# Kernel optimization log

Measured on AMD Instinct MI355X. Metric: run time of the kernel, lower is better.

Reference implementation:

```python
import jax, jax.numpy as jnp
import numpy as np

B, S, D, H = 4, 2048, 1024, 16
DH = D // H  # head dim = 64
MASK_VALUE = -1000000.0


def setup_inputs() -> dict:
    key = jax.random.key(0)
    ks = jax.random.split(key, 8)
    return {
        "key": jax.random.normal(ks[0], (B, S, D), jnp.float32),
        "query": jax.random.normal(ks[1], (B, S, D), jnp.float32),
        "value": jax.random.normal(ks[2], (B, S, D), jnp.float32),
        "valid_lens": jax.random.randint(ks[3], (B,), 0, 2048, jnp.int32),
        # nn.Linear weights stored as [out_features, in_features]
        "Wk": jax.random.normal(ks[4], (D, D), jnp.float32) / np.sqrt(D),
        "Wq": jax.random.normal(ks[5], (D, D), jnp.float32) / np.sqrt(D),
        "Wv": jax.random.normal(ks[6], (D, D), jnp.float32) / np.sqrt(D),
        "Wo": jax.random.normal(ks[7], (D, D), jnp.float32) / np.sqrt(D),
    }


def _split_heads(x):
    # [B, S, D] -> [B, H, S, DH]
    return x.reshape(B, S, H, DH).transpose(0, 2, 1, 3)


def reference(key, query, value, valid_lens, Wk, Wq, Wv, Wo):
    # projections (Linear: x @ W^T, bias=False)
    q = _split_heads(query @ Wq.T)  # [B, H, S, DH]
    k = _split_heads(key @ Wk.T)
    v = _split_heads(value @ Wv.T)

    scale = 1.0 / jnp.sqrt(jnp.asarray(DH, q.dtype))
    scores = jnp.einsum("bhqd,bhkd->bhqk", q, k) * scale  # [B, H, S, S]

    # valid_lens masks the key axis per batch element (same for all heads/queries)
    key_mask = jnp.arange(S) < valid_lens[:, None]  # [B, S]
    scores = jnp.where(key_mask[:, None, None, :], scores, MASK_VALUE)

    attn = jax.nn.softmax(scores, axis=-1)
    out = jnp.einsum("bhqk,bhkd->bhqd", attn, v)  # [B, H, S, DH]
    out = out.transpose(0, 2, 1, 3).reshape(B, S, D)  # concat heads
    return out @ Wo.T
```

## Files before the change

### kernel.cpp

```cpp
#include <hip/hip_runtime.h>
#include <hip/hip_bf16.h>
#include <stdint.h>

typedef __bf16 bf16;
typedef __bf16 bf16x4 __attribute__((ext_vector_type(4)));
typedef __bf16 bf16x8 __attribute__((ext_vector_type(8)));
typedef float f32x4 __attribute__((ext_vector_type(4)));
typedef float f32x8 __attribute__((ext_vector_type(8)));

#define MFMA16 __builtin_amdgcn_mfma_f32_16x16x32_bf16

__device__ __forceinline__ void gload_lds16(void* lds, const void* g) {
  __builtin_amdgcn_global_load_lds(
      (const __attribute__((address_space(1))) unsigned int*)g,
      (__attribute__((address_space(3))) unsigned int*)lds, 16, 0, 0);
}
__device__ __forceinline__ void gload_lds4(void* lds, const void* g) {
  __builtin_amdgcn_global_load_lds(
      (const __attribute__((address_space(1))) unsigned int*)g,
      (__attribute__((address_space(3))) unsigned int*)lds, 4, 0, 0);
}

#define S_BARRIER() __builtin_amdgcn_s_barrier()
#define SCHED_FENCE() __builtin_amdgcn_sched_barrier(0)
#define WAIT_LGKM0()                                   \
  do {                                                 \
    asm volatile("s_waitcnt lgkmcnt(0)" ::: "memory"); \
    __builtin_amdgcn_sched_barrier(0);                 \
  } while (0)
#define WAIT_VM(n) asm volatile("s_waitcnt vmcnt(" #n ")" ::: "memory")

__global__ __launch_bounds__(256) void cvt3(
    const float* __restrict__ s0, const float* __restrict__ s1,
    const float* __restrict__ s2, bf16* __restrict__ d0,
    bf16* __restrict__ d1, bf16* __restrict__ d2) {
  const float* srcs[3] = {s0, s1, s2};
  bf16* dsts[3] = {d0, d1, d2};
  const float* src = srcs[blockIdx.y];
  bf16* dst = dsts[blockIdx.y];
  int i = (blockIdx.x * 256 + threadIdx.x) * 4;
  f32x4 v = *(const f32x4*)(src + i);
  bf16x4 o;
#pragma unroll
  for (int j = 0; j < 4; j++) o[j] = (bf16)v[j];
  *(bf16x4*)(dst + i) = o;
}

__global__ __launch_bounds__(256) void cvt1(const float* __restrict__ src,
                                            bf16* __restrict__ dst) {
  int i = (blockIdx.x * 256 + threadIdx.x) * 4;
  f32x4 v = *(const f32x4*)(src + i);
  bf16x4 o;
#pragma unroll
  for (int j = 0; j < 4; j++) o[j] = (bf16)v[j];
  *(bf16x4*)(dst + i) = o;
}

__global__ __launch_bounds__(256) void cvt4(const float* __restrict__ w0,
                                            const float* __restrict__ w1,
                                            const float* __restrict__ w2,
                                            const float* __restrict__ w3,
                                            bf16* __restrict__ dst) {
  const float* srcs[4] = {w0, w1, w2, w3};
  const float* src = srcs[blockIdx.y];
  int i = (blockIdx.x * 256 + threadIdx.x) * 4;
  f32x4 v = *(const f32x4*)(src + i);
  bf16x4 o;
#pragma unroll
  for (int j = 0; j < 4; j++) o[j] = (bf16)v[j];
  *(bf16x4*)(dst + (size_t)blockIdx.y * 1048576 + i) = o;
}

__device__ __forceinline__ void gemmF_body(const bf16* __restrict__ A,
                                           const bf16* __restrict__ W,
                                           void* __restrict__ Craw, int mode,
                                           int m0, int n0, bf16* smem) {
  constexpr int K = 1024;
  const int t = threadIdx.x;
  const int lane = t & 63;
  const int m16 = lane & 15;
  const int quad = (lane >> 4) & 3;
  const int sw = m16 & 7;
  const int w = t >> 6;
  const int wm = (w >> 2) * 64;
  const int wn = (w & 3) * 64;

  const bf16* Ab = A + (size_t)m0 * K;
  const bf16* Bb = W + (size_t)n0 * K;

  auto STG = [&](int buf, int kt) {
    bf16* dA = smem + buf * 24576;
    bf16* dB = dA + 8192;
    const bf16* sA = Ab + kt * 64;
    const bf16* sB = Bb + kt * 64;
#pragma unroll
    for (int ld = 0; ld < 2; ld++) {
      int idx = ld * 512 + t;
      int row = idx >> 3;
      int c = (idx & 7) ^ (row & 7);
      gload_lds16(dA + idx * 8, sA + (size_t)row * K + c * 8);
    }
#pragma unroll
    for (int ld = 0; ld < 4; ld++) {
      int idx = ld * 512 + t;
      int row = idx >> 3;
      int c = (idx & 7) ^ (row & 7);
      gload_lds16(dB + idx * 8, sB + (size_t)row * K + c * 8);
    }
  };

  bf16x8 aR[8], bR[8];
  auto LD = [&](int buf) {
    const bf16* As = smem + buf * 24576;
    const bf16* Bs = As + 8192;
#pragma unroll
    for (int f = 0; f < 4; f++)
#pragma unroll
      for (int ks = 0; ks < 2; ks++) {
        aR[f * 2 + ks] = *(const bf16x8*)&As[(wm + f * 16 + m16) * 64 +
                                             (((ks * 4 + quad) ^ sw) * 8)];
        bR[f * 2 + ks] = *(const bf16x8*)&Bs[(wn + f * 16 + m16) * 64 +
                                             (((ks * 4 + quad) ^ sw) * 8)];
      }
  };

  f32x4 acc[4][4];
#pragma unroll
  for (int f = 0; f < 4; f++)
#pragma unroll
    for (int g = 0; g < 4; g++) acc[f][g] = (f32x4){0.f, 0.f, 0.f, 0.f};

  auto MM = [&]() {
    __builtin_amdgcn_s_setprio(1);
#pragma unroll
    for (int f = 0; f < 4; f++)
#pragma unroll
      for (int g = 0; g < 4; g++)
#pragma unroll
        for (int ks = 0; ks < 2; ks++)
          acc[f][g] = MFMA16(aR[f * 2 + ks], bR[g * 2 + ks], acc[f][g], 0, 0, 0);
    __builtin_amdgcn_s_setprio(0);
  };

  STG(0, 0);
  STG(1, 1);
  WAIT_VM(6);
  S_BARRIER();

  int bufR = 0;
#pragma unroll 1
  for (int kt = 0; kt < 14; ++kt) {
    LD(bufR);
    int bufS = bufR + 2;
    if (bufS >= 3) bufS -= 3;
    STG(bufS, kt + 2);
    S_BARRIER();
    WAIT_LGKM0();
    MM();
    WAIT_VM(6);
    S_BARRIER();
    bufR = (bufR + 1 == 3) ? 0 : bufR + 1;
  }
  LD(bufR);
  S_BARRIER();
  WAIT_LGKM0();
  MM();
  WAIT_VM(0);
  S_BARRIER();
  bufR = (bufR + 1 == 3) ? 0 : bufR + 1;
  LD(bufR);
  S_BARRIER();
  WAIT_LGKM0();
  MM();

#pragma unroll
  for (int f = 0; f < 4; f++) {
    int rbase = m0 + wm + f * 16 + quad * 4;
#pragma unroll
    for (int g = 0; g < 4; g++) {
      int col = n0 + wn + g * 16 + m16;
#pragma unroll
      for (int r = 0; r < 4; r++) {
        int row = rbase + r;
        if (mode == 0) {
          ((float*)Craw)[(size_t)row * 1024 + col] = acc[f][g][r];
        } else {
          int b = row >> 11, s = row & 2047;
          int h = col >> 6, d = col & 63;
          bf16 v = (bf16)acc[f][g][r];
          if (mode == 1)
            ((bf16*)Craw)[(((size_t)(b * 16 + h)) * 2048 + s) * 64 + d] = v;
          else
            ((bf16*)Craw)[(((size_t)(b * 16 + h)) * 64 + d) * 2048 + s] = v;
        }
      }
    }
  }
}

__global__ __launch_bounds__(512, 2) void gemm_qkv(
    const bf16* __restrict__ xq, const bf16* __restrict__ xk,
    const bf16* __restrict__ xv, const bf16* __restrict__ wb,
    const int* __restrict__ vlen, bf16* __restrict__ qp,
    bf16* __restrict__ kp, bf16* __restrict__ vt) {
  __shared__ bf16 smem[73728];
  const int m0 = blockIdx.y * 128;
  const int n0 = blockIdx.x * 256;
  const int z = blockIdx.z;
  if (z >= 1) {
    int b = m0 >> 11;
    int s0 = m0 & 2047;
    int vl = vlen[b];
    if (vl != 0 && s0 >= vl) return;
  }
  const bf16* A = (z == 0) ? xq : (z == 1) ? xk : xv;
  const bf16* W = wb + (size_t)z * 1048576;
  bf16* C = (z == 0) ? qp : (z == 1) ? kp : vt;
  gemmF_body(A, W, C, (z == 2) ? 2 : 1, m0, n0, smem);
}

__global__ __launch_bounds__(512, 2) void gemm_one(const bf16* __restrict__ A,
                                                   const bf16* __restrict__ W,
                                                   void* __restrict__ Craw,
                                                   int mode) {
  __shared__ bf16 smem[73728];
  gemmF_body(A, W, Craw, mode, blockIdx.y * 128, blockIdx.x * 256, smem);
}

template <int AF32, int WF32>
__global__ __launch_bounds__(256) void gemm_bt(const void* __restrict__ Araw,
                                               const void* __restrict__ Wraw,
                                               void* __restrict__ Craw,
                                               int mode) {
  constexpr int K = 1024;
  __shared__ bf16 As[128 * 32];
  __shared__ bf16 Bs[128 * 32];
  const int t = threadIdx.x;
  const int lane = t & 63;
  const int quad = lane >> 4;
  const int m16 = lane & 15;
  const int w = t >> 6;
  const int m0 = blockIdx.y * 128;
  const int n0 = blockIdx.x * 128;
  const int wm = (w >> 1) * 64;
  const int wn = (w & 1) * 64;

  f32x4 acc[4][4];
#pragma unroll
  for (int i = 0; i < 4; i++)
#pragma unroll
    for (int j = 0; j < 4; j++) acc[i][j] = (f32x4){0.f, 0.f, 0.f, 0.f};

  for (int kt = 0; kt < K / 32; kt++) {
    bf16x8 aR[2], bR[2];
#pragma unroll
    for (int p = 0; p < 2; p++) {
      int idx = p * 256 + t;
      int row = idx >> 2;
      int ce = (idx & 3) * 8;
      size_t aoff = (size_t)(m0 + row) * K + kt * 32 + ce;
      size_t boff = (size_t)(n0 + row) * K + kt * 32 + ce;
      if constexpr (AF32) {
        f32x8 av = *(const f32x8*)((const float*)Araw + aoff);
#pragma unroll
        for (int j = 0; j < 8; j++) aR[p][j] = (bf16)av[j];
      } else {
        aR[p] = *(const bf16x8*)((const bf16*)Araw + aoff);
      }
      if constexpr (WF32) {
        f32x8 bv = *(const f32x8*)((const float*)Wraw + boff);
#pragma unroll
        for (int j = 0; j < 8; j++) bR[p][j] = (bf16)bv[j];
      } else {
        bR[p] = *(const bf16x8*)((const bf16*)Wraw + boff);
      }
    }
    __syncthreads();
#pragma unroll
    for (int p = 0; p < 2; p++) {
      int idx = p * 256 + t;
      *(bf16x8*)&As[idx * 8] = aR[p];
      *(bf16x8*)&Bs[idx * 8] = bR[p];
    }
    __syncthreads();

    bf16x8 af[4], bfr[4];
#pragma unroll
    for (int i = 0; i < 4; i++) {
      af[i] = *(const bf16x8*)&As[(wm + i * 16 + m16) * 32 + quad * 8];
      bfr[i] = *(const bf16x8*)&Bs[(wn + i * 16 + m16) * 32 + quad * 8];
    }
#pragma unroll
    for (int i = 0; i < 4; i++)
#pragma unroll
      for (int j = 0; j < 4; j++)
        acc[i][j] = MFMA16(af[i], bfr[j], acc[i][j], 0, 0, 0);
  }

#pragma unroll
  for (int i = 0; i < 4; i++) {
    int rbase = m0 + wm + i * 16 + quad * 4;
#pragma unroll
    for (int j = 0; j < 4; j++) {
      int col = n0 + wn + j * 16 + m16;
#pragma unroll
      for (int r = 0; r < 4; r++) {
        int row = rbase + r;
        if (mode == 0) {
          ((float*)Craw)[(size_t)row * 1024 + col] = acc[i][j][r];
        } else {
          int b = row >> 11, s = row & 2047;
          int h = col >> 6, d = col & 63;
          bf16 v = (bf16)acc[i][j][r];
          if (mode == 1)
            ((bf16*)Craw)[(((size_t)(b * 16 + h)) * 2048 + s) * 64 + d] = v;
          else
            ((bf16*)Craw)[(((size_t)(b * 16 + h)) * 64 + d) * 2048 + s] = v;
        }
      }
    }
  }
}

__global__ __launch_bounds__(512, 2) void attn(const bf16* __restrict__ qp,
                                               const bf16* __restrict__ kp,
                                               const bf16* __restrict__ vt,
                                               const int* __restrict__ vlen,
                                               bf16* __restrict__ ctx) {
  __shared__ bf16 Ks[2][4096];
  __shared__ bf16 Vs[2][4096];

  const int t = threadIdx.x;
  const int lane = t & 63;
  const int quad = (lane >> 4) & 3;
  const int m16 = lane & 15;
  const int sw = m16 & 7;
  const int w = t >> 6;
  const int id = blockIdx.y * 8 + blockIdx.x;
  const int xcd = id & 7;
  const int j = id >> 3;
  const int bh = (j >> 3) * 8 + xcd;
  const int qt = j & 7;
  const int b = bh >> 4;
  const int h = bh & 15;
  const int vl = vlen[b];

  const float C1 = 0.18033688f;
  const float C2 = 46.166241f;
  const float sC1 = (vl == 0) ? 0.0f : C1;
  const float sC2 = (vl == 0) ? 0.0f : C2;

  bf16x8 qf[2][2];
#pragma unroll
  for (int a = 0; a < 2; a++) {
    const bf16* qb =
        qp + ((size_t)(bh * 2048 + qt * 256 + w * 32 + a * 16 + m16)) * 64;
    qf[a][0] = *(const bf16x8*)(qb + quad * 8);
    qf[a][1] = *(const bf16x8*)(qb + 32 + quad * 8);
  }

  float rsum[2] = {0.f, 0.f};
  f32x4 o[2][4];
#pragma unroll
  for (int a = 0; a < 2; a++)
#pragma unroll
    for (int nt = 0; nt < 4; nt++) o[a][nt] = (f32x4){0.f, 0.f, 0.f, 0.f};

  const int ktEnd = (vl == 0) ? 32 : ((vl + 63) >> 6);

  const int krow = t >> 3;
  const int kgc = (t & 7) ^ (krow & 7);
  auto STAGE = [&](int buf, int kt2) {
    gload_lds16(&Ks[buf][t * 8],
                &kp[((size_t)(bh * 2048 + kt2 * 64 + krow)) * 64 + kgc * 8]);
#pragma unroll
    for (int ld = 0; ld < 4; ld++) {
      int c = ld * 512 + t;
      int dh = c >> 5;
      int i4 = c & 31;
      int c8 = i4 >> 2;
      int jw = i4 & 3;
      int lc = c8 ^ (dh & 7);
      int slot = lc * 8 + jw * 2;
      int ks2 = slot >> 5;
      int w32 = slot & 31;
      int key = ks2 * 32 + ((w32 >> 2) & 1) * 16 + (w32 >> 3) * 4 + (w32 & 3);
      gload_lds4(&Vs[buf][c * 2],
                 &vt[((size_t)(bh * 64 + dh)) * 2048 + kt2 * 64 + key]);
    }
  };

  STAGE(0, 0);

  for (int kt = 0; kt < ktEnd; kt++) {
    const int cur = kt & 1;
    if (kt + 1 < ktEnd) {
      STAGE(cur ^ 1, kt + 1);
      WAIT_VM(5);
    } else {
      WAIT_VM(0);
    }
    S_BARRIER();
    SCHED_FENCE();
    const bf16* Ksb = Ks[cur];
    const bf16* Vsb = Vs[cur];

    f32x4 s[2][4];
#pragma unroll
    for (int a = 0; a < 2; a++)
#pragma unroll
      for (int nt = 0; nt < 4; nt++) s[a][nt] = (f32x4){0.f, 0.f, 0.f, 0.f};
#pragma unroll
    for (int nt = 0; nt < 4; nt++) {
#pragma unroll
      for (int ks = 0; ks < 2; ks++) {
        bf16x8 kf = *(const bf16x8*)&Ksb[(nt * 16 + m16) * 64 +
                                         (((ks * 4 + quad) ^ sw) * 8)];
        s[0][nt] = MFMA16(kf, qf[0][ks], s[0][nt], 0, 0, 0);
        s[1][nt] = MFMA16(kf, qf[1][ks], s[1][nt], 0, 0, 0);
      }
    }

    bf16x8 pa[2][2];
    const bool partial = (vl != 0) && (kt == (vl >> 6));
    if (!partial) {
#pragma unroll
      for (int a = 0; a < 2; a++)
#pragma unroll
        for (int nt = 0; nt < 4; nt++)
#pragma unroll
          for (int r = 0; r < 4; r++) {
            float p = __builtin_amdgcn_exp2f(s[a][nt][r] * sC1 - sC2);
            bf16 pb = (bf16)p;
            rsum[a] += (float)pb;
            pa[a][nt >> 1][(nt & 1) * 4 + r] = pb;
          }
    } else {
#pragma unroll
      for (int a = 0; a < 2; a++)
#pragma unroll
        for (int nt = 0; nt < 4; nt++) {
          int keyb = kt * 64 + nt * 16 + quad * 4;
#pragma unroll
          for (int r = 0; r < 4; r++) {
            float arg = (keyb + r >= vl) ? -12800.0f
                                         : (s[a][nt][r] * sC1 - sC2);
            float p = __builtin_amdgcn_exp2f(arg);
            bf16 pb = (bf16)p;
            rsum[a] += (float)pb;
            pa[a][nt >> 1][(nt & 1) * 4 + r] = pb;
          }
        }
    }

#pragma unroll
    for (int ks = 0; ks < 2; ks++) {
#pragma unroll
      for (int nt = 0; nt < 4; nt++) {
        bf16x8 vf = *(const bf16x8*)&Vsb[(nt * 16 + m16) * 64 +
                                         (((ks * 4 + quad) ^ sw) * 8)];
        o[0][nt] = MFMA16(pa[0][ks], vf, o[0][nt], 0, 0, 0);
        o[1][nt] = MFMA16(pa[1][ks], vf, o[1][nt], 0, 0, 0);
      }
    }
    S_BARRIER();
    SCHED_FENCE();
  }

#pragma unroll
  for (int a = 0; a < 2; a++) {
    rsum[a] += __shfl_xor(rsum[a], 16);
    rsum[a] += __shfl_xor(rsum[a], 32);
    rsum[a] = 1.0f / rsum[a];
  }

#pragma unroll
  for (int a = 0; a < 2; a++) {
#pragma unroll
    for (int r = 0; r < 4; r++) {
      float rr = __shfl(rsum[a], (lane & 48) | (quad * 4 + r));
#pragma unroll
      for (int nt = 0; nt < 4; nt++) {
        int dh = nt * 16 + m16;
        int sr = qt * 256 + w * 32 + a * 16 + quad * 4 + r;
        ctx[((size_t)(b * 2048 + sr)) * 1024 + h * 64 + dh] =
            (bf16)(o[a][nt][r] * rr);
      }
    }
  }
}

extern "C" void kernel_launch(void* const* d_in, const int* in_sizes, int n_in,
                              void* d_out, int out_size, void* d_ws,
                              size_t ws_size, hipStream_t stream) {
  const float* key = (const float*)d_in[0];
  const float* query = (const float*)d_in[1];
  const float* value = (const float*)d_in[2];
  const int* vlen = (const int*)d_in[3];
  const float* Wk = (const float*)d_in[4];
  const float* Wq = (const float*)d_in[5];
  const float* Wv = (const float*)d_in[6];
  const float* Wo = (const float*)d_in[7];

  const size_t NE = (size_t)4 * 2048 * 1024;
  const size_t WE = 1048576;

  const size_t needA = (6 * NE + 4 * WE) * sizeof(bf16);
  const size_t needB = (5 * NE + 4 * WE) * sizeof(bf16);
  dim3 gg(4, 64), gb(512), cb(256), ag(8, 64), ab(512);

  if (ws_size >= needA) {
    bf16* qp = (bf16*)d_ws;
    bf16* kp = qp + NE;
    bf16* vt = kp + NE;
    bf16* xq = vt + NE;
    bf16* xk = xq + NE;
    bf16* xv = xk + NE;
    bf16* wb = xv + NE;
    bf16* ctx = xq;

    cvt4<<<dim3(1024, 4), cb, 0, stream>>>(Wq, Wk, Wv, Wo, wb);
    cvt3<<<dim3(8192, 3), cb, 0, stream>>>(query, key, value, xq, xk, xv);
    gemm_qkv<<<dim3(4, 64, 3), gb, 0, stream>>>(xq, xk, xv, wb, vlen, qp, kp,
                                                vt);
    attn<<<ag, ab, 0, stream>>>(qp, kp, vt, vlen, ctx);
    gemm_one<<<gg, gb, 0, stream>>>(ctx, wb + 3 * WE, d_out, 0);
  } else if (ws_size >= needB) {
    bf16* qp = (bf16*)d_ws;
    bf16* kp = qp + NE;
    bf16* vt = kp + NE;
    bf16* ctx = vt + NE;
    bf16* xb = ctx + NE;
    bf16* wb = xb + NE;

    cvt4<<<dim3(1024, 4), cb, 0, stream>>>(Wq, Wk, Wv, Wo, wb);
    cvt1<<<8192, cb, 0, stream>>>(query, xb);
    gemm_one<<<gg, gb, 0, stream>>>(xb, wb + 0 * WE, qp, 1);
    cvt1<<<8192, cb, 0, stream>>>(key, xb);
    gemm_one<<<gg, gb, 0, stream>>>(xb, wb + 1 * WE, kp, 1);
    cvt1<<<8192, cb, 0, stream>>>(value, xb);
    gemm_one<<<gg, gb, 0, stream>>>(xb, wb + 2 * WE, vt, 2);
    attn<<<ag, ab, 0, stream>>>(qp, kp, vt, vlen, ctx);
    gemm_one<<<gg, gb, 0, stream>>>(ctx, wb + 3 * WE, d_out, 0);
  } else {
    bf16* qp = (bf16*)d_ws;
    bf16* kp = qp + NE;
    bf16* vt = kp + NE;
    bf16* ctx = vt + NE;
    dim3 g8(8, 64), b256(256);
    gemm_bt<1, 1><<<g8, b256, 0, stream>>>(query, Wq, qp, 1);
    gemm_bt<1, 1><<<g8, b256, 0, stream>>>(key, Wk, kp, 1);
    gemm_bt<1, 1><<<g8, b256, 0, stream>>>(value, Wv, vt, 2);
    attn<<<ag, ab, 0, stream>>>(qp, kp, vt, vlen, ctx);
    gemm_bt<0, 1><<<g8, b256, 0, stream>>>(ctx, Wo, d_out, 0);
  }
}
```

Before: 334.0 us.

## Triple-buffer K/V tiles, software-pipeline QK^T with softmax/PV, vectorize V staging

The attention kernel moves from double to triple LDS buffering and stages the next-next tile while it runs QK^T for tile kt+1 interleaved with the softmax and PV of tile kt, so MFMA work overlaps the exp computation. V staging drops the sixteen 4-byte global-to-LDS loads per thread in favor of one 16-byte load with XOR swizzling. PV then rebuilds each V fragment from two 4-element LDS reads. LDS use grows by half and register pressure rises from holding two score sets, which could hurt occupancy at launch_bounds(512,2).

```diff
diff --git a/kernel.cpp b/kernel.cpp
--- a/kernel.cpp
+++ b/kernel.cpp
@@ -14,11 +14,6 @@
   __builtin_amdgcn_global_load_lds(
       (const __attribute__((address_space(1))) unsigned int*)g,
       (__attribute__((address_space(3))) unsigned int*)lds, 16, 0, 0);
-}
-__device__ __forceinline__ void gload_lds4(void* lds, const void* g) {
-  __builtin_amdgcn_global_load_lds(
-      (const __attribute__((address_space(1))) unsigned int*)g,
-      (__attribute__((address_space(3))) unsigned int*)lds, 4, 0, 0);
 }
 
 #define S_BARRIER() __builtin_amdgcn_s_barrier()
@@ -327,8 +322,8 @@
                                                const bf16* __restrict__ vt,
                                                const int* __restrict__ vlen,
                                                bf16* __restrict__ ctx) {
-  __shared__ bf16 Ks[2][4096];
-  __shared__ bf16 Vs[2][4096];
+  __shared__ bf16 Ks[3][4096];
+  __shared__ bf16 Vs[3][4096];
 
   const int t = threadIdx.x;
   const int lane = t & 63;
@@ -338,17 +333,15 @@
   const int w = t >> 6;
   const int id = blockIdx.y * 8 + blockIdx.x;
   const int xcd = id & 7;
-  const int j = id >> 3;
-  const int bh = (j >> 3) * 8 + xcd;
-  const int qt = j & 7;
+  const int jj = id >> 3;
+  const int bh = (jj >> 3) * 8 + xcd;
+  const int qt = jj & 7;
   const int b = bh >> 4;
   const int h = bh & 15;
   const int vl = vlen[b];
 
-  const float C1 = 0.18033688f;
-  const float C2 = 46.166241f;
-  const float sC1 = (vl == 0) ? 0.0f : C1;
-  const float sC2 = (vl == 0) ? 0.0f : C2;
+  const float sC1 = (vl == 0) ? 0.0f : 0.18033688f;
+  const float sC2 = (vl == 0) ? 0.0f : 46.166241f;
 
   bf16x8 qf[2][2];
 #pragma unroll
@@ -368,60 +361,35 @@
 
   const int ktEnd = (vl == 0) ? 32 : ((vl + 63) >> 6);
 
-  const int krow = t >> 3;
-  const int kgc = (t & 7) ^ (krow & 7);
+  const int srow = t >> 3;
+  const int sgc = (t & 7) ^ (srow & 7);
   auto STAGE = [&](int buf, int kt2) {
     gload_lds16(&Ks[buf][t * 8],
-                &kp[((size_t)(bh * 2048 + kt2 * 64 + krow)) * 64 + kgc * 8]);
-#pragma unroll
-    for (int ld = 0; ld < 4; ld++) {
-      int c = ld * 512 + t;
-      int dh = c >> 5;
-      int i4 = c & 31;
-      int c8 = i4 >> 2;
-      int jw = i4 & 3;
-      int lc = c8 ^ (dh & 7);
-      int slot = lc * 8 + jw * 2;
-      int ks2 = slot >> 5;
-      int w32 = slot & 31;
-      int key = ks2 * 32 + ((w32 >> 2) & 1) * 16 + (w32 >> 3) * 4 + (w32 & 3);
-      gload_lds4(&Vs[buf][c * 2],
-                 &vt[((size_t)(bh * 64 + dh)) * 2048 + kt2 * 64 + key]);
-    }
-  };
-
-  STAGE(0, 0);
-
-  for (int kt = 0; kt < ktEnd; kt++) {
-    const int cur = kt & 1;
-    if (kt + 1 < ktEnd) {
-      STAGE(cur ^ 1, kt + 1);
-      WAIT_VM(5);
-    } else {
-      WAIT_VM(0);
-    }
-    S_BARRIER();
-    SCHED_FENCE();
-    const bf16* Ksb = Ks[cur];
-    const bf16* Vsb = Vs[cur];
-
-    f32x4 s[2][4];
+                &kp[((size_t)(bh * 2048 + kt2 * 64 + srow)) * 64 + sgc * 8]);
+    gload_lds16(&Vs[buf][t * 8],
+                &vt[((size_t)(bh * 64 + srow)) * 2048 + kt2 * 64 + sgc * 8]);
+  };
+
+  f32x4 s[2][4], sN[2][4];
+
+  auto QKT = [&](int buf, f32x4 (&sv)[2][4]) {
 #pragma unroll
     for (int a = 0; a < 2; a++)
 #pragma unroll
-      for (int nt = 0; nt < 4; nt++) s[a][nt] = (f32x4){0.f, 0.f, 0.f, 0.f};
+      for (int nt = 0; nt < 4; nt++) sv[a][nt] = (f32x4){0.f, 0.f, 0.f, 0.f};
 #pragma unroll
     for (int nt = 0; nt < 4; nt++) {
 #pragma unroll
       for (int ks = 0; ks < 2; ks++) {
-        bf16x8 kf = *(const bf16x8*)&Ksb[(nt * 16 + m16) * 64 +
-                                         (((ks * 4 + quad) ^ sw) * 8)];
-        s[0][nt] = MFMA16(kf, qf[0][ks], s[0][nt], 0, 0, 0);
-        s[1][nt] = MFMA16(kf, qf[1][ks], s[1][nt], 0, 0, 0);
-      }
-    }
-
-    bf16x8 pa[2][2];
+        bf16x8 kf = *(const bf16x8*)&Ks[buf][(nt * 16 + m16) * 64 +
+                                            (((ks * 4 + quad) ^ sw) * 8)];
+        sv[0][nt] = MFMA16(kf, qf[0][ks], sv[0][nt], 0, 0, 0);
+        sv[1][nt] = MFMA16(kf, qf[1][ks], sv[1][nt], 0, 0, 0);
+      }
+    }
+  };
+
+  auto SOFTMAX = [&](int kt, bf16x8 (&pa)[2][2]) {
     const bool partial = (vl != 0) && (kt == (vl >> 6));
     if (!partial) {
 #pragma unroll
@@ -443,8 +411,8 @@
           int keyb = kt * 64 + nt * 16 + quad * 4;
 #pragma unroll
           for (int r = 0; r < 4; r++) {
-            float arg = (keyb + r >= vl) ? -12800.0f
-                                         : (s[a][nt][r] * sC1 - sC2);
+            float arg =
+                (keyb + r >= vl) ? -12800.0f : (s[a][nt][r] * sC1 - sC2);
             float p = __builtin_amdgcn_exp2f(arg);
             bf16 pb = (bf16)p;
             rsum[a] += (float)pb;
@@ -452,19 +420,65 @@
           }
         }
     }
-
+  };
+
+  auto PV = [&](int buf, bf16x8 (&pa)[2][2]) {
 #pragma unroll
     for (int ks = 0; ks < 2; ks++) {
 #pragma unroll
       for (int nt = 0; nt < 4; nt++) {
-        bf16x8 vf = *(const bf16x8*)&Vsb[(nt * 16 + m16) * 64 +
-                                         (((ks * 4 + quad) ^ sw) * 8)];
+        int row = nt * 16 + m16;
+        int base = row * 64;
+        int glo = ks * 4 + (quad >> 1);
+        int q8 = (quad & 1) * 4;
+        bf16x4 lo = *(const bf16x4*)&Vs[buf][base + ((glo ^ (row & 7)) * 8) + q8];
+        bf16x4 hi =
+            *(const bf16x4*)&Vs[buf][base + (((glo + 2) ^ (row & 7)) * 8) + q8];
+        bf16x8 vf = __builtin_shufflevector(lo, hi, 0, 1, 2, 3, 4, 5, 6, 7);
         o[0][nt] = MFMA16(pa[0][ks], vf, o[0][nt], 0, 0, 0);
         o[1][nt] = MFMA16(pa[1][ks], vf, o[1][nt], 0, 0, 0);
       }
     }
-    S_BARRIER();
-    SCHED_FENCE();
+  };
+
+  STAGE(0, 0);
+  WAIT_VM(0);
+  S_BARRIER();
+  SCHED_FENCE();
+  QKT(0, s);
+  if (ktEnd > 1) STAGE(1, 1);
+
+  int bCur = 0;
+#pragma unroll 1
+  for (int kt = 0; kt < ktEnd; kt++) {
+    int bNext = bCur + 1;
+    if (bNext == 3) bNext = 0;
+    int bStage = bNext + 1;
+    if (bStage == 3) bStage = 0;
+    const bool hasNext = (kt + 1 < ktEnd);
+    if (kt + 2 < ktEnd) {
+      STAGE(bStage, kt + 2);
+      WAIT_VM(2);
+    } else if (hasNext) {
+      WAIT_VM(0);
+    }
+    if (hasNext) {
+      S_BARRIER();
+      SCHED_FENCE();
+    }
+    bf16x8 pa[2][2];
+    SOFTMAX(kt, pa);
+    if (hasNext) QKT(bNext, sN);
+    PV(bCur, pa);
+    if (hasNext) {
+      S_BARRIER();
+      SCHED_FENCE();
+#pragma unroll
+      for (int a = 0; a < 2; a++)
+#pragma unroll
+        for (int nt = 0; nt < 4; nt++) s[a][nt] = sN[a][nt];
+    }
+    bCur = bNext;
   }
 
 #pragma unroll
```

Result: no change. 336.5 us (+0.7%).

## Pre-permute V^T in GEMM epilogue and use 16-byte LDS loads; shrink attention blocks

Applied to the files above, without the earlier changes.

The QKV GEMM epilogue now writes V^T with the key permutation the attention MFMA expects. This lets the attention kernel stage V with 16-byte global-to-LDS loads instead of many 4-byte loads with per-element index math. The attention kernel also moves to 256-thread blocks of 128 queries with twice as many blocks, four blocks per CU, and 16-byte loads for both K and V. This cuts load instruction count and address arithmetic and raises block-level parallelism. In exchange, K/V tiles are loaded from global memory twice as often, and the scattered V^T stores are permuted.

```diff
diff --git a/kernel.cpp b/kernel.cpp
--- a/kernel.cpp
+++ b/kernel.cpp
@@ -14,11 +14,6 @@
   __builtin_amdgcn_global_load_lds(
       (const __attribute__((address_space(1))) unsigned int*)g,
       (__attribute__((address_space(3))) unsigned int*)lds, 16, 0, 0);
-}
-__device__ __forceinline__ void gload_lds4(void* lds, const void* g) {
-  __builtin_amdgcn_global_load_lds(
-      (const __attribute__((address_space(1))) unsigned int*)g,
-      (__attribute__((address_space(3))) unsigned int*)lds, 4, 0, 0);
 }
 
 #define S_BARRIER() __builtin_amdgcn_s_barrier()
@@ -29,6 +24,12 @@
     __builtin_amdgcn_sched_barrier(0);                 \
   } while (0)
 #define WAIT_VM(n) asm volatile("s_waitcnt vmcnt(" #n ")" ::: "memory")
+
+__device__ __forceinline__ int vperm(int s) {
+  int s6 = s & 63;
+  return (s & ~63) | (s6 & 32) | (((s6 >> 2) & 3) << 3) |
+         (((s6 >> 4) & 1) << 2) | (s6 & 3);
+}
 
 __global__ __launch_bounds__(256) void cvt3(
     const float* __restrict__ s0, const float* __restrict__ s1,
@@ -191,7 +192,8 @@
           if (mode == 1)
             ((bf16*)Craw)[(((size_t)(b * 16 + h)) * 2048 + s) * 64 + d] = v;
           else
-            ((bf16*)Craw)[(((size_t)(b * 16 + h)) * 64 + d) * 2048 + s] = v;
+            ((bf16*)Craw)[(((size_t)(b * 16 + h)) * 64 + d) * 2048 + vperm(s)] =
+                v;
         }
       }
     }
@@ -315,14 +317,15 @@
           if (mode == 1)
             ((bf16*)Craw)[(((size_t)(b * 16 + h)) * 2048 + s) * 64 + d] = v;
           else
-            ((bf16*)Craw)[(((size_t)(b * 16 + h)) * 64 + d) * 2048 + s] = v;
+            ((bf16*)Craw)[(((size_t)(b * 16 + h)) * 64 + d) * 2048 + vperm(s)] =
+                v;
         }
       }
     }
   }
 }
 
-__global__ __launch_bounds__(512, 2) void attn(const bf16* __restrict__ qp,
+__global__ __launch_bounds__(256, 4) void attn(const bf16* __restrict__ qp,
                                                const bf16* __restrict__ kp,
                                                const bf16* __restrict__ vt,
                                                const int* __restrict__ vlen,
@@ -338,23 +341,21 @@
   const int w = t >> 6;
   const int id = blockIdx.y * 8 + blockIdx.x;
   const int xcd = id & 7;
-  const int j = id >> 3;
-  const int bh = (j >> 3) * 8 + xcd;
-  const int qt = j & 7;
+  const int jj = id >> 3;
+  const int bh = (jj >> 4) * 8 + xcd;
+  const int qt = jj & 15;
   const int b = bh >> 4;
   const int h = bh & 15;
   const int vl = vlen[b];
 
-  const float C1 = 0.18033688f;
-  const float C2 = 46.166241f;
-  const float sC1 = (vl == 0) ? 0.0f : C1;
-  const float sC2 = (vl == 0) ? 0.0f : C2;
+  const float sC1 = (vl == 0) ? 0.0f : 0.18033688f;
+  const float sC2 = (vl == 0) ? 0.0f : 46.166241f;
 
   bf16x8 qf[2][2];
 #pragma unroll
   for (int a = 0; a < 2; a++) {
     const bf16* qb =
-        qp + ((size_t)(bh * 2048 + qt * 256 + w * 32 + a * 16 + m16)) * 64;
+        qp + ((size_t)(bh * 2048 + qt * 128 + w * 32 + a * 16 + m16)) * 64;
     qf[a][0] = *(const bf16x8*)(qb + quad * 8);
     qf[a][1] = *(const bf16x8*)(qb + 32 + quad * 8);
   }
@@ -368,42 +369,38 @@
 
   const int ktEnd = (vl == 0) ? 32 : ((vl + 63) >> 6);
 
-  const int krow = t >> 3;
-  const int kgc = (t & 7) ^ (krow & 7);
   auto STAGE = [&](int buf, int kt2) {
-    gload_lds16(&Ks[buf][t * 8],
-                &kp[((size_t)(bh * 2048 + kt2 * 64 + krow)) * 64 + kgc * 8]);
-#pragma unroll
-    for (int ld = 0; ld < 4; ld++) {
-      int c = ld * 512 + t;
-      int dh = c >> 5;
-      int i4 = c & 31;
-      int c8 = i4 >> 2;
-      int jw = i4 & 3;
-      int lc = c8 ^ (dh & 7);
-      int slot = lc * 8 + jw * 2;
-      int ks2 = slot >> 5;
-      int w32 = slot & 31;
-      int key = ks2 * 32 + ((w32 >> 2) & 1) * 16 + (w32 >> 3) * 4 + (w32 & 3);
-      gload_lds4(&Vs[buf][c * 2],
-                 &vt[((size_t)(bh * 64 + dh)) * 2048 + kt2 * 64 + key]);
+#pragma unroll
+    for (int ld = 0; ld < 2; ld++) {
+      int idx = ld * 256 + t;
+      int row = idx >> 3;
+      int gc = (idx & 7) ^ (row & 7);
+      gload_lds16(&Ks[buf][idx * 8],
+                  &kp[((size_t)(bh * 2048 + kt2 * 64 + row)) * 64 + gc * 8]);
+    }
+#pragma unroll
+    for (int ld = 0; ld < 2; ld++) {
+      int idx = ld * 256 + t;
+      int row = idx >> 3;
+      int gc = (idx & 7) ^ (row & 7);
+      gload_lds16(&Vs[buf][idx * 8],
+                  &vt[((size_t)(bh * 64 + row)) * 2048 + kt2 * 64 + gc * 8]);
     }
   };
 
   STAGE(0, 0);
 
+#pragma unroll 1
   for (int kt = 0; kt < ktEnd; kt++) {
     const int cur = kt & 1;
     if (kt + 1 < ktEnd) {
       STAGE(cur ^ 1, kt + 1);
-      WAIT_VM(5);
+      WAIT_VM(4);
     } else {
       WAIT_VM(0);
     }
     S_BARRIER();
     SCHED_FENCE();
-    const bf16* Ksb = Ks[cur];
-    const bf16* Vsb = Vs[cur];
 
     f32x4 s[2][4];
 #pragma unroll
@@ -414,8 +411,8 @@
     for (int nt = 0; nt < 4; nt++) {
 #pragma unroll
       for (int ks = 0; ks < 2; ks++) {
-        bf16x8 kf = *(const bf16x8*)&Ksb[(nt * 16 + m16) * 64 +
-                                         (((ks * 4 + quad) ^ sw) * 8)];
+        bf16x8 kf = *(const bf16x8*)&Ks[cur][(nt * 16 + m16) * 64 +
+                                            (((ks * 4 + quad) ^ sw) * 8)];
         s[0][nt] = MFMA16(kf, qf[0][ks], s[0][nt], 0, 0, 0);
         s[1][nt] = MFMA16(kf, qf[1][ks], s[1][nt], 0, 0, 0);
       }
@@ -443,8 +440,8 @@
           int keyb = kt * 64 + nt * 16 + quad * 4;
 #pragma unroll
           for (int r = 0; r < 4; r++) {
-            float arg = (keyb + r >= vl) ? -12800.0f
-                                         : (s[a][nt][r] * sC1 - sC2);
+            float arg =
+                (keyb + r >= vl) ? -12800.0f : (s[a][nt][r] * sC1 - sC2);
             float p = __builtin_amdgcn_exp2f(arg);
             bf16 pb = (bf16)p;
             rsum[a] += (float)pb;
@@ -457,8 +454,8 @@
     for (int ks = 0; ks < 2; ks++) {
 #pragma unroll
       for (int nt = 0; nt < 4; nt++) {
-        bf16x8 vf = *(const bf16x8*)&Vsb[(nt * 16 + m16) * 64 +
-                                         (((ks * 4 + quad) ^ sw) * 8)];
+        bf16x8 vf = *(const bf16x8*)&Vs[cur][(nt * 16 + m16) * 64 +
+                                            (((ks * 4 + quad) ^ sw) * 8)];
         o[0][nt] = MFMA16(pa[0][ks], vf, o[0][nt], 0, 0, 0);
         o[1][nt] = MFMA16(pa[1][ks], vf, o[1][nt], 0, 0, 0);
       }
@@ -482,7 +479,7 @@
 #pragma unroll
       for (int nt = 0; nt < 4; nt++) {
         int dh = nt * 16 + m16;
-        int sr = qt * 256 + w * 32 + a * 16 + quad * 4 + r;
+        int sr = qt * 128 + w * 32 + a * 16 + quad * 4 + r;
         ctx[((size_t)(b * 2048 + sr)) * 1024 + h * 64 + dh] =
             (bf16)(o[a][nt][r] * rr);
       }
@@ -507,7 +504,7 @@
 
   const size_t needA = (6 * NE + 4 * WE) * sizeof(bf16);
   const size_t needB = (5 * NE + 4 * WE) * sizeof(bf16);
-  dim3 gg(4, 64), gb(512), cb(256), ag(8, 64), ab(512);
+  dim3 gg(4, 64), gb(512), cb(256), ag(8, 128), ab(256);
 
   if (ws_size >= needA) {
     bf16* qp = (bf16*)d_ws;
```

Result: faster. 325.5 us (-2.5%).
